# Kernel tuning notes

Measured on AMD Instinct MI355X. Metric: run time of the kernel, lower is better.

The kernel has to match this reference:

```python
import jax, jax.numpy as jnp
import numpy as np

B, S, V, HD, HID, ND = 32, 32, 100, 32, 64, 10


def setup_inputs() -> dict:
    key = jax.random.key(0)
    ks = jax.random.split(key, 32)
    gaps = jax.random.uniform(ks[0], (B, S), jnp.float32) * 0.1 + 0.01
    batch_train_time = jnp.cumsum(gaps, axis=1)                      # sorted event times
    batch_train_type = jax.random.randint(ks[1], (B, S), 0, V)       # event marks in [0, V)
    batch_train_mask = jnp.ones((B, S), jnp.float32)

    def lin(k, i, o):
        return jax.random.normal(k, (i, o), jnp.float32) * (1.0 / np.sqrt(i))

    inp = dict(batch_train_time=batch_train_time,
               batch_train_type=batch_train_type,
               batch_train_mask=batch_train_mask,
               logits=jnp.zeros((2, V * V), jnp.float32),            # torch init: zeros
               h0=jax.random.normal(ks[2], (V, HD), jnp.float32) * 0.01,
               # drift f: in = h_dim + diff_t + last_t
               fW1=lin(ks[3], HD + 2, HID), fb1=jnp.zeros((HID,)),
               fW2=lin(ks[4], HID, HID), fb2=jnp.zeros((HID,)),
               fW3=lin(ks[5], HID, HD), fb3=jnp.zeros((HD,)),
               # diffusion g: in = h_dim + diff_t
               gW1=lin(ks[6], HD + 1, HID), gb1=jnp.zeros((HID,)),
               gW2=lin(ks[7], HID, HID), gb2=jnp.zeros((HID,)),
               gW3=lin(ks[8], HID, HD), gb3=jnp.zeros((HD,)),
               # intensity e: h -> softplus scalar per vertex
               eW1=lin(ks[9], HD, HID), eb1=jnp.zeros((HID,)),
               eW2=lin(ks[10], HID, 1), eb2=jnp.zeros((1,)),
               # jump h
               jW1=lin(ks[11], HD, HID), jb1=jnp.zeros((HID,)),
               jW2=lin(ks[12], HID, HD), jb2=jnp.zeros((HD,)),
               # A_MSG edge mlp: [h_send, h_recv] -> message
               mW1=lin(ks[13], 2 * HD, HID), mb1=jnp.zeros((HID,)),
               mW2=lin(ks[14], HID, HD), mb2=jnp.zeros((HD,)))
    return inp


def reference(batch_train_time, batch_train_type, batch_train_mask, logits, h0,
              fW1, fb1, fW2, fb2, fW3, fb3,
              gW1, gb1, gW2, gb2, gW3, gb3,
              eW1, eb1, eW2, eb2, jW1, jb1, jW2, jb2, mW1, mb1, mW2, mb2):
    barange = jnp.arange(B)
    edge_prob = jax.nn.softmax(logits, axis=0)[1]  # [V*V], P(edge present)

    def mlp3(x, W1, b1, W2, b2, W3, b3):
        h = jnp.tanh(x @ W1 + b1)
        h = jnp.tanh(h @ W2 + b2)
        return h @ W3 + b3

    def f_drift(h, dft, last):
        return mlp3(jnp.concatenate([h, dft, last], -1), fW1, fb1, fW2, fb2, fW3, fb3)

    def g_diff(h, dft):
        return mlp3(jnp.concatenate([h, dft], -1), gW1, gb1, gW2, gb2, gW3, gb3)

    def e_int(h):  # [B,V,HD] -> [B,V] positive intensity
        return jax.nn.softplus(jnp.tanh(h @ eW1 + eb1) @ eW2 + eb2)[..., 0]

    def jump(h):
        return jnp.tanh(h @ jW1 + jb1) @ jW2 + jb2

    def msg_jump(h, ev):
        # message passing from the event node to every vertex, gated by edge_prob
        send = h[barange, ev]                                          # [B,HD]
        pair = jnp.concatenate([jnp.broadcast_to(send[:, None, :], h.shape), h], -1)
        m = jnp.tanh(pair @ mW1 + mb1) @ mW2 + mb2                     # [B,V,HD]
        p = edge_prob[ev[:, None] * V + jnp.arange(V)[None, :]]        # [B,V]
        h = h + m * p[:, :, None]
        # jump update at the event node
        he = h[barange, ev]
        return h.at[barange, ev].add(jump(he))

    def euler(h, t0, t1, key):
        dt = (t1 - t0) / ND                                            # [B]
        dtb = dt[:, None, None]
        l_init = e_int(h)

        def step(carry, j):
            h, k = carry
            k, sub = jax.random.split(k)
            noise = jax.random.normal(sub, h.shape, h.dtype)
            dft = jnp.broadcast_to(dtb * (j + 1.0), (B, V, 1))
            last = jnp.broadcast_to(t0[:, None, None], (B, V, 1))
            h = h + f_drift(h, dft, last) * dtb + g_diff(h, dft) * jnp.sqrt(dtb) * noise
            return (h, k), e_int(h)

        (h, key), ls = jax.lax.scan(step, (h, key), jnp.arange(ND, dtype=jnp.float32))
        l_ts = jnp.concatenate([l_init[:, :, None], jnp.moveaxis(ls, 0, 2)], axis=2)  # [B,V,ND+1]
        ts = t0[:, None] + dt[:, None] * jnp.arange(ND + 1, dtype=dt.dtype)           # [B,ND+1]
        return h, key, ts, l_ts

    # t = 0: initial intensity + first jump
    h = jnp.broadcast_to(h0[None], (B, V, HD))
    l0 = e_int(h)
    ev0 = batch_train_type[:, 0]
    lt0 = l0[barange, ev0]
    h = msg_jump(h, ev0)
    key = jax.random.key(42)

    def interval(carry, xs):
        h, key = carry
        t0, t1, ev = xs
        h, key, ts, l_ts = euler(h, t0, t1, key)
        l_last = l_ts[:, :, -1]                 # pre-jump (left) intensities
        lt = l_last[barange, ev]
        h = msg_jump(h, ev)
        return (h, key), (ts, l_ts, l_last, lt)

    xs = (batch_train_time[:, :-1].T, batch_train_time[:, 1:].T, batch_train_type[:, 1:].T)
    (_h, _k), (ts_all, lts_all, llast_all, lt_all) = jax.lax.scan(interval, (h, key), xs)

    tsave = jnp.moveaxis(ts_all, 0, 1).reshape(B, -1)                       # [B,(S-1)*(ND+1)]
    a_l_tsave = jnp.transpose(lts_all, (1, 2, 0, 3)).reshape(B, V, -1)      # [B,V,(S-1)*(ND+1)]
    a_l_batch_l = jnp.concatenate([l0[:, None, :], jnp.moveaxis(llast_all, 0, 1)], axis=1)  # [B,S,V]
    a_l_time_l = jnp.concatenate([lt0[:, None], lt_all.T], axis=1)          # [B,S]

    sum_term = jnp.sum(jnp.log(a_l_time_l + 1e-16) * batch_train_mask)
    em = jnp.repeat(batch_train_mask[:, 1:], ND + 1, axis=1)                # [B,(S-1)*(ND+1)]
    em = jnp.broadcast_to(em[:, None, :], a_l_tsave.shape)
    lts = a_l_tsave * em
    dts = jnp.diff(tsave, axis=1)[:, None, :]
    integral = jnp.sum((lts[:, :, :-1] * em[:, :, :-1] + lts[:, :, 1:] * em[:, :, 1:])
                       * (dts * em[:, :, 1:])) / 2
    a_nll = integral - sum_term
    return a_nll, a_l_batch_l
```

## Files before the change

### kernel.cpp

```cpp
#include <hip/hip_runtime.h>
#include <hip/hip_fp16.h>
#include <stdint.h>

#define B_  32
#define S_  32
#define V_  100
#define HD_ 32
#define HID_ 64
#define ND_ 10
#define NROW (B_*V_)
#define NTILE 7
#define NBLK (B_*NTILE)
#define NFRAG 58

#define WO_EP    14848
#define WO_HA    24848
#define WO_HB    127248
#define WO_ACC   229648
#define WO_PREVL 232848
#define WO_PREVT 236048
#define WO_LTLOG 239248
#define WO_NOISE 240272
#define NOISE_FLOATS ((size_t)310 * NBLK * 64 * 8)

typedef __attribute__((ext_vector_type(8))) _Float16 f16x8;
typedef __attribute__((ext_vector_type(4))) float f32x4;

#define LGKM_FENCE asm volatile("s_waitcnt lgkmcnt(0)" ::: "memory")

__host__ __device__ inline void tf2x32(uint32_t k0, uint32_t k1,
                                       uint32_t& x0, uint32_t& x1) {
  uint32_t ks0 = k0, ks1 = k1, ks2 = k0 ^ k1 ^ 0x1BD11BDAu;
#define TFR(r) { x0 += x1; x1 = (x1 << (r)) | (x1 >> (32 - (r))); x1 ^= x0; }
  x0 += ks0; x1 += ks1;
  TFR(13) TFR(15) TFR(26) TFR(6)
  x0 += ks1; x1 += ks2 + 1u;
  TFR(17) TFR(29) TFR(16) TFR(24)
  x0 += ks2; x1 += ks0 + 2u;
  TFR(13) TFR(15) TFR(26) TFR(6)
  x0 += ks0; x1 += ks1 + 3u;
  TFR(17) TFR(29) TFR(16) TFR(24)
  x0 += ks1; x1 += ks2 + 4u;
  TFR(13) TFR(15) TFR(26) TFR(6)
  x0 += ks2; x1 += ks0 + 5u;
#undef TFR
}

__device__ __forceinline__ float erfinv_f(float x) {
  float w = -log1pf(-x * x);
  float p;
  if (w < 5.0f) {
    w -= 2.5f;
    p = 2.81022636e-08f;
    p = fmaf(p, w, 3.43273939e-07f);
    p = fmaf(p, w, -3.5233877e-06f);
    p = fmaf(p, w, -4.39150654e-06f);
    p = fmaf(p, w, 0.00021858087f);
    p = fmaf(p, w, -0.00125372503f);
    p = fmaf(p, w, -0.00417768164f);
    p = fmaf(p, w, 0.246640727f);
    p = fmaf(p, w, 1.50140941f);
  } else {
    w = sqrtf(w) - 3.0f;
    p = -0.000200214257f;
    p = fmaf(p, w, 0.000100950558f);
    p = fmaf(p, w, 0.00134934322f);
    p = fmaf(p, w, -0.00367342844f);
    p = fmaf(p, w, 0.00573950773f);
    p = fmaf(p, w, -0.0076224613f);
    p = fmaf(p, w, 0.00943887047f);
    p = fmaf(p, w, 1.00167406f);
    p = fmaf(p, w, 2.83297682f);
  }
  return p * x;
}

__device__ __forceinline__ float tanh_e(float x) {
  float e = __builtin_amdgcn_exp2f(x * 2.885390082f);
  return 1.0f - 2.0f * __builtin_amdgcn_rcpf(e + 1.0f);
}
__device__ __forceinline__ float softplus_fast(float x) {
  return fmaxf(x, 0.0f) + __logf(1.0f + __expf(-fabsf(x)));
}
__device__ __forceinline__ unsigned short f16b(float x) {
  __half h = __float2half(x);
  return *reinterpret_cast<unsigned short*>(&h);
}
__device__ __forceinline__ uint32_t pk2(float a, float b) {
  return (uint32_t)f16b(a) | ((uint32_t)f16b(b) << 16);
}
__device__ __forceinline__ f32x4 MF(f16x8 a, f16x8 b, f32x4 c) {
  return __builtin_amdgcn_mfma_f32_16x16x32_f16(a, b, c, 0, 0, 0);
}

struct SubK { uint32_t k[ND_][2]; };
struct AllK { uint32_t k[310][2]; };

__device__ __forceinline__ void noise8(int row0, int lane, uint32_t k0, uint32_t k1,
                                       float* n) {
  int g = lane >> 4, li = lane & 15;
#pragma unroll
  for (int v = 0; v < 8; ++v) {
    int reg = v & 3, t = v >> 2;
    int row = row0 + 4 * g + reg;
    uint32_t x0 = 0u, x1 = (uint32_t)(row * HD_ + li + 16 * t);
    tf2x32(k0, k1, x0, x1);
    uint32_t bits = x0 ^ x1;
    float fr = __uint_as_float(0x3f800000u | (bits >> 9)) - 1.0f;
    const float LOW = -0.99999994f;
    float u = fmaxf(LOW, fr * 2.0f + LOW);
    n[v] = 1.4142135f * erfinv_f(u);
  }
}

__global__ void prep_k(const float* __restrict__ fW1, const float* __restrict__ gW1,
                       const float* __restrict__ fW2, const float* __restrict__ gW2,
                       const float* __restrict__ fW3, const float* __restrict__ gW3,
                       const float* __restrict__ eW1, const float* __restrict__ eW2,
                       const float* __restrict__ mW1, const float* __restrict__ mW2,
                       const float* __restrict__ jW1, const float* __restrict__ jW2,
                       const float* __restrict__ logits, float* __restrict__ ws) {
  int tid = blockIdx.x * 256 + threadIdx.x;
  if (tid < NFRAG * 64) {
    int fid = tid >> 6, lane = tid & 63;
    int g = lane >> 4, li = lane & 15;
    const float* src; int k0 = 0, n0 = 0, ncol = HID_; bool hperm = false, col0 = false;
    if (fid < 4)       { src = fW1; n0 = 16 * fid;       hperm = true; }
    else if (fid < 8)  { src = gW1; n0 = 16 * (fid - 4); hperm = true; }
    else if (fid < 16) { int q = fid - 8;  src = fW2; n0 = 16 * (q >> 1); k0 = 32 * (q & 1); }
    else if (fid < 24) { int q = fid - 16; src = gW2; n0 = 16 * (q >> 1); k0 = 32 * (q & 1); }
    else if (fid < 28) { int q = fid - 24; src = fW3; n0 = 16 * (q >> 1); k0 = 32 * (q & 1); ncol = HD_; }
    else if (fid < 32) { int q = fid - 28; src = gW3; n0 = 16 * (q >> 1); k0 = 32 * (q & 1); ncol = HD_; }
    else if (fid < 36) { src = eW1; n0 = 16 * (fid - 32); hperm = true; }
    else if (fid < 38) { src = eW2; k0 = 32 * (fid - 36); col0 = true; }
    else if (fid < 46) { int q = fid - 38; src = mW1; k0 = 32 * (q >> 2); n0 = 16 * (q & 3); hperm = true; }
    else if (fid < 50) { int q = fid - 46; src = mW2; k0 = 32 * (q >> 1); n0 = 16 * (q & 1); ncol = HD_; }
    else if (fid < 54) { src = jW1; n0 = 16 * (fid - 50); hperm = true; }
    else               { int q = fid - 54; src = jW2; k0 = 32 * (q >> 1); n0 = 16 * (q & 1); ncol = HD_; }
    unsigned short v[8];
#pragma unroll
    for (int j = 0; j < 8; ++j) {
      int sl = 8 * g + j;
      int k;
      if (hperm) k = k0 + ((sl >> 1) + 16 * (sl & 1));
      else { int s2 = k0 + sl; k = (s2 >> 2) + 16 * (s2 & 3); }
      float x;
      if (col0) x = (li == 0) ? src[k] : 0.0f;
      else      x = src[k * ncol + (n0 + li)];
      v[j] = f16b(x);
    }
    uint4 o;
    o.x = (uint32_t)v[0] | ((uint32_t)v[1] << 16);
    o.y = (uint32_t)v[2] | ((uint32_t)v[3] << 16);
    o.z = (uint32_t)v[4] | ((uint32_t)v[5] << 16);
    o.w = (uint32_t)v[6] | ((uint32_t)v[7] << 16);
    ((uint4*)ws)[fid * 64 + lane] = o;
  } else if (tid < NFRAG * 64 + V_ * V_) {
    int idx = tid - NFRAG * 64;
    float l0v = logits[idx], l1v = logits[V_ * V_ + idx];
    float mx = fmaxf(l0v, l1v);
    float e0 = expf(l0v - mx), e1 = expf(l1v - mx);
    ws[WO_EP + idx] = e1 / (e0 + e1);
  }
}

__global__ void noise_k(float* __restrict__ np, AllK ak) {
  int pair = blockIdx.x * 4 + (threadIdx.x >> 6);
  int lane = threadIdx.x & 63;
  int sg = pair / NBLK, bid = pair - sg * NBLK;
  int b = bid / NTILE, tile = bid - b * NTILE;
  int row0 = b * V_ + tile * 16;
  float n[8];
  noise8(row0, lane, ak.k[sg][0], ak.k[sg][1], n);
  float* dst = np + ((size_t)pair * 64 + lane) * 8;
  f32x4 a = {n[0], n[1], n[2], n[3]}, c = {n[4], n[5], n[6], n[7]};
  ((f32x4*)dst)[0] = a;
  ((f32x4*)dst)[1] = c;
}

template<int K4, int O>
__device__ __forceinline__ float dotWxT(const float* __restrict__ W,
                                        const float* __restrict__ x,
                                        float a, int lane) {
#pragma unroll
  for (int kb = 0; kb < K4; ++kb) {
    float4 xv = *(const float4*)(x + kb * 4);
    a = fmaf(xv.x, W[(kb * 4 + 0) * O + lane], a);
    a = fmaf(xv.y, W[(kb * 4 + 1) * O + lane], a);
    a = fmaf(xv.z, W[(kb * 4 + 2) * O + lane], a);
    a = fmaf(xv.w, W[(kb * 4 + 3) * O + lane], a);
  }
  return a;
}

__launch_bounds__(256)
__global__ void init_k(const int* __restrict__ type_, const float* __restrict__ mask_,
                       const float* __restrict__ h0,
                       const float* __restrict__ eW1, const float* __restrict__ eb1,
                       const float* __restrict__ eW2, const float* __restrict__ eb2,
                       float* __restrict__ hA, float* __restrict__ acc,
                       float* __restrict__ ltlog, float* __restrict__ dout) {
  __shared__ float xls[4][64];
  const int w = threadIdx.x >> 6, lane = threadIdx.x & 63;
  const int row = blockIdx.x * 4 + w;
  const int b = row / V_, v = row - b * V_;
  if (lane < 32) {
    float x = h0[v * HD_ + lane];
    xls[w][lane] = x;
    hA[row * HD_ + lane] = x;
  }
  float a = dotWxT<8, 64>(eW1, xls[w], eb1[lane], lane);
  float t = tanhf(a) * eW2[lane];
#pragma unroll
  for (int o = 1; o < 64; o <<= 1) t += __shfl_xor(t, o, 64);
  float z = t + eb2[0];
  float l0 = fmaxf(z, 0.0f) + log1pf(expf(-fabsf(z)));
  if (lane == 0) {
    dout[1 + (b * S_ + 0) * V_ + v] = l0;
    acc[row] = 0.0f;
    if (v == type_[b * S_]) ltlog[b] = logf(l0 + 1e-16f) * mask_[b * S_];
  }
}

__launch_bounds__(64, 1)
__global__ void euler_k(const float* __restrict__ time_, const int* __restrict__ type_,
                        const float* __restrict__ mask_, const float* __restrict__ wsf,
                        const float* __restrict__ fb1, const float* __restrict__ fb2,
                        const float* __restrict__ fb3, const float* __restrict__ gb1,
                        const float* __restrict__ gb2, const float* __restrict__ gb3,
                        const float* __restrict__ eb1, const float* __restrict__ eb2,
                        const float* __restrict__ eW2, const float* __restrict__ fW1,
                        const float* __restrict__ gW1,
                        const float* __restrict__ mb1, const float* __restrict__ mb2,
                        const float* __restrict__ jb1, const float* __restrict__ jb2,
                        const float* __restrict__ hsrc, float* __restrict__ hdst,
                        float* __restrict__ acc, float* __restrict__ prevl,
                        float* __restrict__ prevt, float* __restrict__ ltlog,
                        float* __restrict__ dout,
                        const float* __restrict__ nin, int s, SubK skc) {
  __shared__ unsigned short actF[16 * 72];
  __shared__ unsigned short actG[16 * 72];
  __shared__ unsigned short hTl[16 * 40];
  __shared__ f16x8 wl[12 * 64];

  const int lane = threadIdx.x;
  const int g = lane >> 4, li = lane & 15;
  const int bid = blockIdx.x;
  const int b = bid / NTILE, tile = bid - b * NTILE;
  const int row0 = b * V_ + tile * 16;
  const int rmax = b * V_ + (V_ - 1);
  const int ev = type_[b * S_ + s - 1];

  const f16x8* WBv = (const f16x8*)wsf;
  const float* ep = wsf + WO_EP;

#pragma unroll
  for (int i = 0; i < 8; ++i) wl[i * 64 + lane] = WBv[i * 64 + lane];
#pragma unroll
  for (int i = 0; i < 4; ++i) wl[(8 + i) * 64 + lane] = WBv[(32 + i) * 64 + lane];

  f16x8 w2f[8], w2g[8], w3f[4], w3g[4];
#pragma unroll
  for (int i = 0; i < 8; ++i) w2f[i] = WBv[(8 + i) * 64 + lane];
#pragma unroll
  for (int i = 0; i < 8; ++i) w2g[i] = WBv[(16 + i) * 64 + lane];
#pragma unroll
  for (int i = 0; i < 4; ++i) w3f[i] = WBv[(24 + i) * 64 + lane];
#pragma unroll
  for (int i = 0; i < 4; ++i) w3g[i] = WBv[(28 + i) * 64 + lane];

  float fb1v[4], gb1v[4], fb2v[4], gb2v[4], eb1v[4], e2v[4], fw32[4], fw33[4], gw32[4];
  float mb1v[4], jb1v[4];
#pragma unroll
  for (int nt = 0; nt < 4; ++nt) {
    int n = li + 16 * nt;
    fb1v[nt] = fb1[n]; gb1v[nt] = gb1[n];
    fb2v[nt] = fb2[n]; gb2v[nt] = gb2[n];
    eb1v[nt] = eb1[n]; e2v[nt] = eW2[n];
    fw32[nt] = fW1[32 * HID_ + n]; fw33[nt] = fW1[33 * HID_ + n];
    gw32[nt] = gW1[32 * HID_ + n];
    mb1v[nt] = mb1[n]; jb1v[nt] = jb1[n];
  }
  float fb3v[2], gb3v[2], mb2v[2], jb2v[2];
#pragma unroll
  for (int nt = 0; nt < 2; ++nt) {
    fb3v[nt] = fb3[li + 16 * nt]; gb3v[nt] = gb3[li + 16 * nt];
    mb2v[nt] = mb2[li + 16 * nt]; jb2v[nt] = jb2[li + 16 * nt];
  }
  const float eb2v = eb2[0];

  const float t0 = time_[b * S_ + s - 1], t1 = time_[b * S_ + s];
  const float dt = (t1 - t0) / 10.0f;
  const float sq = sqrtf(dt);
  const float msk = mask_[b * S_ + s], mskp = mask_[b * S_ + s - 1];

  float hv[2][4];
#pragma unroll
  for (int t = 0; t < 2; ++t)
#pragma unroll
    for (int reg = 0; reg < 4; ++reg) {
      int rv = row0 + 4 * g + reg; if (rv > rmax) rv = rmax;
      hv[t][reg] = hsrc[rv * HD_ + li + 16 * t];
    }

  {
    float sd0 = hsrc[(b * V_ + ev) * HD_ + li];
    float sd1 = hsrc[(b * V_ + ev) * HD_ + li + 16];
    uint32_t su = pk2(sd0, sd1);
#pragma unroll
    for (int reg = 0; reg < 4; ++reg) {
      *(uint32_t*)&actF[(4 * g + reg) * 72 + 2 * li] = su;
      *(uint32_t*)&actG[(4 * g + reg) * 72 + 2 * li] = pk2(hv[0][reg], hv[1][reg]);
    }
    LGKM_FENCE;
    f16x8 ap0 = *(const f16x8*)&actF[li * 72 + 8 * g];
    f16x8 ap1 = *(const f16x8*)&actG[li * 72 + 8 * g];
    f32x4 cm[4];
#pragma unroll
    for (int nt = 0; nt < 4; ++nt) {
      f32x4 c = {mb1v[nt], mb1v[nt], mb1v[nt], mb1v[nt]};
      c = MF(ap0, WBv[(38 + nt) * 64 + lane], c);
      cm[nt] = MF(ap1, WBv[(42 + nt) * 64 + lane], c);
    }
#pragma unroll
    for (int reg = 0; reg < 4; ++reg) {
      uint2 u;
      u.x = pk2(tanh_e(cm[0][reg]), tanh_e(cm[1][reg]));
      u.y = pk2(tanh_e(cm[2][reg]), tanh_e(cm[3][reg]));
      *(uint2*)&actF[(4 * g + reg) * 72 + 4 * li] = u;
    }
    LGKM_FENCE;
    f16x8 am0 = *(const f16x8*)&actF[li * 72 + 8 * g];
    f16x8 am1 = *(const f16x8*)&actF[li * 72 + 32 + 8 * g];
    f32x4 mm[2];
#pragma unroll
    for (int nt = 0; nt < 2; ++nt) {
      f32x4 c = {mb2v[nt], mb2v[nt], mb2v[nt], mb2v[nt]};
      c = MF(am0, WBv[(46 + nt) * 64 + lane], c);
      mm[nt] = MF(am1, WBv[(48 + nt) * 64 + lane], c);
    }
#pragma unroll
    for (int reg = 0; reg < 4; ++reg) {
      int v = tile * 16 + 4 * g + reg; int vc = (v < V_) ? v : (V_ - 1);
      float p = ep[ev * V_ + vc];
      hv[0][reg] += mm[0][reg] * p;
      hv[1][reg] += mm[1][reg] * p;
    }
    if (tile == (ev >> 4)) {
#pragma unroll
      for (int reg = 0; reg < 4; ++reg)
        *(uint32_t*)&hTl[(4 * g + reg) * 40 + 2 * li] = pk2(hv[0][reg], hv[1][reg]);
      LGKM_FENCE;
      f16x8 ah = *(const f16x8*)&hTl[li * 40 + 8 * g];
      f32x4 cj[4];
#pragma unroll
      for (int nt = 0; nt < 4; ++nt) {
        f32x4 c = {jb1v[nt], jb1v[nt], jb1v[nt], jb1v[nt]};
        cj[nt] = MF(ah, WBv[(50 + nt) * 64 + lane], c);
      }
#pragma unroll
      for (int reg = 0; reg < 4; ++reg) {
        uint2 u;
        u.x = pk2(tanh_e(cj[0][reg]), tanh_e(cj[1][reg]));
        u.y = pk2(tanh_e(cj[2][reg]), tanh_e(cj[3][reg]));
        *(uint2*)&actG[(4 * g + reg) * 72 + 4 * li] = u;
      }
      LGKM_FENCE;
      f16x8 aj0 = *(const f16x8*)&actG[li * 72 + 8 * g];
      f16x8 aj1 = *(const f16x8*)&actG[li * 72 + 32 + 8 * g];
      f32x4 jm[2];
#pragma unroll
      for (int nt = 0; nt < 2; ++nt) {
        f32x4 c = {jb2v[nt], jb2v[nt], jb2v[nt], jb2v[nt]};
        c = MF(aj0, WBv[(54 + nt) * 64 + lane], c);
        jm[nt] = MF(aj1, WBv[(56 + nt) * 64 + lane], c);
      }
#pragma unroll
      for (int reg = 0; reg < 4; ++reg)
        if (tile * 16 + 4 * g + reg == ev) {
          hv[0][reg] += jm[0][reg];
          hv[1][reg] += jm[1][reg];
        }
    }
#pragma unroll
    for (int reg = 0; reg < 4; ++reg)
      *(uint32_t*)&hTl[(4 * g + reg) * 40 + 2 * li] = pk2(hv[0][reg], hv[1][reg]);
    LGKM_FENCE;
  }

  float accv[4], lprev[4], plv[4];
#pragma unroll
  for (int reg = 0; reg < 4; ++reg) {
    int rv = row0 + 4 * g + reg; if (rv > rmax) rv = rmax;
    accv[reg] = acc[rv];
    plv[reg] = (s > 1) ? prevl[rv] : 0.0f;
  }
  const float ptv = (s > 1) ? prevt[row0] : 0.0f;

  auto efin = [&](f32x4* ce, float* lout) {
#pragma unroll
    for (int reg = 0; reg < 4; ++reg) {
      float p = tanh_e(ce[0][reg]) * e2v[0];
      p = fmaf(tanh_e(ce[1][reg]), e2v[1], p);
      p = fmaf(tanh_e(ce[2][reg]), e2v[2], p);
      p = fmaf(tanh_e(ce[3][reg]), e2v[3], p);
#pragma unroll
      for (int m = 1; m < 16; m <<= 1) p += __shfl_xor(p, m, 64);
      lout[reg] = softplus_fast(p + eb2v);
    }
  };

#pragma unroll 1
  for (int j = 0; j < ND_; ++j) {
    f32x4 q0, q1;
    if (nin) {
      const float* qp = nin + ((size_t)(j * NBLK + bid) * 64 + lane) * 8;
      q0 = ((const f32x4*)qp)[0]; q1 = ((const f32x4*)qp)[1];
    } else {
      float n[8];
      noise8(row0, lane, skc.k[j][0], skc.k[j][1], n);
      q0 = {n[0], n[1], n[2], n[3]}; q1 = {n[4], n[5], n[6], n[7]};
    }

    f16x8 ah = *(const f16x8*)&hTl[li * 40 + 8 * g];
    f32x4 cf[4], cg[4], ce[4];
#pragma unroll
    for (int nt = 0; nt < 4; ++nt) {
      f32x4 c0 = {fb1v[nt], fb1v[nt], fb1v[nt], fb1v[nt]};
      cf[nt] = MF(ah, wl[nt * 64 + lane], c0);
      f32x4 c1 = {gb1v[nt], gb1v[nt], gb1v[nt], gb1v[nt]};
      cg[nt] = MF(ah, wl[(4 + nt) * 64 + lane], c1);
      f32x4 c2 = {eb1v[nt], eb1v[nt], eb1v[nt], eb1v[nt]};
      ce[nt] = MF(ah, wl[(8 + nt) * 64 + lane], c2);
    }
    const float dft = dt * (float)(j + 1);
    float addf[4], addg[4];
#pragma unroll
    for (int nt = 0; nt < 4; ++nt) {
      addf[nt] = dft * fw32[nt] + t0 * fw33[nt];
      addg[nt] = dft * gw32[nt];
    }
#pragma unroll
    for (int reg = 0; reg < 4; ++reg) {
      uint2 uf, ug;
      uf.x = pk2(tanh_e(cf[0][reg] + addf[0]), tanh_e(cf[1][reg] + addf[1]));
      uf.y = pk2(tanh_e(cf[2][reg] + addf[2]), tanh_e(cf[3][reg] + addf[3]));
      *(uint2*)&actF[(4 * g + reg) * 72 + 4 * li] = uf;
      ug.x = pk2(tanh_e(cg[0][reg] + addg[0]), tanh_e(cg[1][reg] + addg[1]));
      ug.y = pk2(tanh_e(cg[2][reg] + addg[2]), tanh_e(cg[3][reg] + addg[3]));
      *(uint2*)&actG[(4 * g + reg) * 72 + 4 * li] = ug;
    }
    float lc[4];
    efin(ce, lc);
    if (j == 0) {
      if (s > 1) {
#pragma unroll
        for (int reg = 0; reg < 4; ++reg)
          accv[reg] += (plv[reg] * mskp + lc[reg] * msk) * (t0 - ptv) * msk;
      }
    } else {
      float dtm = dt * msk;
#pragma unroll
      for (int reg = 0; reg < 4; ++reg)
        accv[reg] += (lprev[reg] * msk + lc[reg] * msk) * dtm;
    }
#pragma unroll
    for (int reg = 0; reg < 4; ++reg) lprev[reg] = lc[reg];
    LGKM_FENCE;
    f16x8 af0 = *(const f16x8*)&actF[li * 72 + 8 * g];
    f16x8 af1 = *(const f16x8*)&actF[li * 72 + 32 + 8 * g];
    f16x8 ag0 = *(const f16x8*)&actG[li * 72 + 8 * g];
    f16x8 ag1 = *(const f16x8*)&actG[li * 72 + 32 + 8 * g];
#pragma unroll
    for (int nt = 0; nt < 4; ++nt) {
      f32x4 c = {fb2v[nt], fb2v[nt], fb2v[nt], fb2v[nt]};
      c = MF(af0, w2f[2 * nt], c);
      cf[nt] = MF(af1, w2f[2 * nt + 1], c);
      f32x4 d = {gb2v[nt], gb2v[nt], gb2v[nt], gb2v[nt]};
      d = MF(ag0, w2g[2 * nt], d);
      cg[nt] = MF(ag1, w2g[2 * nt + 1], d);
    }
#pragma unroll
    for (int reg = 0; reg < 4; ++reg) {
      uint2 uf, ug;
      uf.x = pk2(tanh_e(cf[0][reg]), tanh_e(cf[1][reg]));
      uf.y = pk2(tanh_e(cf[2][reg]), tanh_e(cf[3][reg]));
      *(uint2*)&actF[(4 * g + reg) * 72 + 4 * li] = uf;
      ug.x = pk2(tanh_e(cg[0][reg]), tanh_e(cg[1][reg]));
      ug.y = pk2(tanh_e(cg[2][reg]), tanh_e(cg[3][reg]));
      *(uint2*)&actG[(4 * g + reg) * 72 + 4 * li] = ug;
    }
    LGKM_FENCE;
    af0 = *(const f16x8*)&actF[li * 72 + 8 * g];
    af1 = *(const f16x8*)&actF[li * 72 + 32 + 8 * g];
    ag0 = *(const f16x8*)&actG[li * 72 + 8 * g];
    ag1 = *(const f16x8*)&actG[li * 72 + 32 + 8 * g];
    f32x4 dr[2], di[2];
#pragma unroll
    for (int nt = 0; nt < 2; ++nt) {
      f32x4 c = {fb3v[nt], fb3v[nt], fb3v[nt], fb3v[nt]};
      c = MF(af0, w3f[2 * nt], c);
      dr[nt] = MF(af1, w3f[2 * nt + 1], c);
      f32x4 d = {gb3v[nt], gb3v[nt], gb3v[nt], gb3v[nt]};
      d = MF(ag0, w3g[2 * nt], d);
      di[nt] = MF(ag1, w3g[2 * nt + 1], d);
    }
#pragma unroll
    for (int reg = 0; reg < 4; ++reg) {
      hv[0][reg] += dr[0][reg] * dt + di[0][reg] * sq * q0[reg];
      hv[1][reg] += dr[1][reg] * dt + di[1][reg] * sq * q1[reg];
    }
#pragma unroll
    for (int reg = 0; reg < 4; ++reg)
      *(uint32_t*)&hTl[(4 * g + reg) * 40 + 2 * li] = pk2(hv[0][reg], hv[1][reg]);
    LGKM_FENCE;
  }

  float llast[4];
  {
    f16x8 ah = *(const f16x8*)&hTl[li * 40 + 8 * g];
    f32x4 ce[4];
#pragma unroll
    for (int nt = 0; nt < 4; ++nt) {
      f32x4 c = {eb1v[nt], eb1v[nt], eb1v[nt], eb1v[nt]};
      ce[nt] = MF(ah, wl[(8 + nt) * 64 + lane], c);
    }
    efin(ce, llast);
    float dtm = dt * msk;
#pragma unroll
    for (int reg = 0; reg < 4; ++reg)
      accv[reg] += (lprev[reg] * msk + llast[reg] * msk) * dtm;
  }

#pragma unroll
  for (int t = 0; t < 2; ++t)
#pragma unroll
    for (int reg = 0; reg < 4; ++reg) {
      int v = tile * 16 + 4 * g + reg;
      if (v < V_) hdst[(row0 + 4 * g + reg) * HD_ + li + 16 * t] = hv[t][reg];
    }
  if (li == 0) {
    int evn = type_[b * S_ + s];
    float pt = t0 + dt * 10.0f;
#pragma unroll
    for (int reg = 0; reg < 4; ++reg) {
      int v = tile * 16 + 4 * g + reg;
      if (v < V_) {
        int rv = row0 + 4 * g + reg;
        acc[rv] = accv[reg];
        prevl[rv] = llast[reg];
        prevt[rv] = pt;
        dout[1 + (b * S_ + s) * V_ + v] = llast[reg];
        if (v == evn) ltlog[s * B_ + b] = logf(llast[reg] + 1e-16f) * msk;
      }
    }
  }
}

__global__ void reduce_k(const float* __restrict__ acc, const float* __restrict__ ltlog,
                         float* __restrict__ dout) {
  __shared__ double sh[512];
  int t = threadIdx.x;
  double ia = 0.0, st = 0.0;
  for (int i = t; i < NROW; i += 256) ia += (double)acc[i];
  for (int i = t; i < B_ * S_; i += 256) st += (double)ltlog[i];
  sh[t] = ia; sh[256 + t] = st;
  __syncthreads();
  for (int o = 128; o > 0; o >>= 1) {
    if (t < o) { sh[t] += sh[t + o]; sh[256 + t] += sh[256 + t + o]; }
    __syncthreads();
  }
  if (t == 0) dout[0] = (float)(0.5 * sh[0] - sh[256]);
}

extern "C" void kernel_launch(void* const* d_in, const int* in_sizes, int n_in,
                              void* d_out, int out_size, void* d_ws, size_t ws_size,
                              hipStream_t stream) {
  const float* time_  = (const float*)d_in[0];
  const int*   type_  = (const int*)d_in[1];
  const float* mask_  = (const float*)d_in[2];
  const float* logits = (const float*)d_in[3];
  const float* h0     = (const float*)d_in[4];
  const float* fW1 = (const float*)d_in[5];  const float* fb1 = (const float*)d_in[6];
  const float* fW2 = (const float*)d_in[7];  const float* fb2 = (const float*)d_in[8];
  const float* fW3 = (const float*)d_in[9];  const float* fb3 = (const float*)d_in[10];
  const float* gW1 = (const float*)d_in[11]; const float* gb1 = (const float*)d_in[12];
  const float* gW2 = (const float*)d_in[13]; const float* gb2 = (const float*)d_in[14];
  const float* gW3 = (const float*)d_in[15]; const float* gb3 = (const float*)d_in[16];
  const float* eW1 = (const float*)d_in[17]; const float* eb1 = (const float*)d_in[18];
  const float* eW2 = (const float*)d_in[19]; const float* eb2 = (const float*)d_in[20];
  const float* jW1 = (const float*)d_in[21]; const float* jb1 = (const float*)d_in[22];
  const float* jW2 = (const float*)d_in[23]; const float* jb2 = (const float*)d_in[24];
  const float* mW1 = (const float*)d_in[25]; const float* mb1 = (const float*)d_in[26];
  const float* mW2 = (const float*)d_in[27]; const float* mb2 = (const float*)d_in[28];
  float* out = (float*)d_out;

  float* ws    = (float*)d_ws;
  float* hA    = ws + WO_HA;
  float* hB    = ws + WO_HB;
  float* acc   = ws + WO_ACC;
  float* prevl = ws + WO_PREVL;
  float* prevt = ws + WO_PREVT;
  float* ltlog = ws + WO_LTLOG;

  uint32_t kh = 0u, kl = 42u;
  AllK ak;
  for (int n = 0; n < 310; ++n) {
    uint32_t a0 = 0u, a1 = 0u; tf2x32(kh, kl, a0, a1);
    uint32_t b0 = 0u, b1 = 1u; tf2x32(kh, kl, b0, b1);
    ak.k[n][0] = b0; ak.k[n][1] = b1;
    kh = a0; kl = a1;
  }

  const bool useNoise = ws_size >= ((size_t)WO_NOISE + NOISE_FLOATS) * 4;
  float* noisep = useNoise ? (ws + WO_NOISE) : nullptr;

  prep_k<<<54, 256, 0, stream>>>(fW1, gW1, fW2, gW2, fW3, gW3, eW1, eW2,
                                 mW1, mW2, jW1, jW2, logits, ws);
  init_k<<<NROW / 4, 256, 0, stream>>>(type_, mask_, h0, eW1, eb1, eW2, eb2,
                                       hA, acc, ltlog, out);
  if (useNoise)
    noise_k<<<(310 * NBLK) / 4, 256, 0, stream>>>(noisep, ak);

  for (int s = 1; s <= 31; ++s) {
    const float* hs = (s & 1) ? hA : hB;
    float*       hd = (s & 1) ? hB : hA;
    SubK skc;
    for (int j = 0; j < ND_; ++j) {
      skc.k[j][0] = ak.k[(s - 1) * ND_ + j][0];
      skc.k[j][1] = ak.k[(s - 1) * ND_ + j][1];
    }
    const float* nin = useNoise ? (noisep + (size_t)(s - 1) * ND_ * NBLK * 64 * 8) : nullptr;
    euler_k<<<NBLK, 64, 0, stream>>>(time_, type_, mask_, ws,
                                     fb1, fb2, fb3, gb1, gb2, gb3, eb1, eb2, eW2,
                                     fW1, gW1, mb1, mb2, jb1, jb2,
                                     hs, hd, acc, prevl, prevt, ltlog, out,
                                     nin, s, skc);
  }
  reduce_k<<<1, 256, 0, stream>>>(acc, ltlog, out);
}
```

Baseline: 1.119 ms.

## Split drift and diffusion MLPs across two waves and generate noise inline

Each euler block now runs two wavefronts: wave 0 evaluates the drift MLP and owns the state update, and wave 1 evaluates the diffusion MLP plus the intensity head and accumulation. Diffusion outputs pass to wave 0 through shared memory, with block barriers each Euler substep. The precomputed noise buffer and its kernel are removed; each wave computes its half of the Threefry/erfinv noise inline. This halves per-wave MFMA and tanh work on the serial critical path, at the cost of two __syncthreads per substep and recomputing RNG inside the timed loop.

```diff
diff --git a/kernel.cpp b/kernel.cpp
--- a/kernel.cpp
+++ b/kernel.cpp
@@ -20,8 +20,6 @@
 #define WO_PREVL 232848
 #define WO_PREVT 236048
 #define WO_LTLOG 239248
-#define WO_NOISE 240272
-#define NOISE_FLOATS ((size_t)310 * NBLK * 64 * 8)
 
 typedef __attribute__((ext_vector_type(8))) _Float16 f16x8;
 typedef __attribute__((ext_vector_type(4))) float f32x4;
@@ -94,14 +92,12 @@
 }
 
 struct SubK { uint32_t k[ND_][2]; };
-struct AllK { uint32_t k[310][2]; };
-
-__device__ __forceinline__ void noise8(int row0, int lane, uint32_t k0, uint32_t k1,
+
+__device__ __forceinline__ void noise4(int row0, int lane, int t, uint32_t k0, uint32_t k1,
                                        float* n) {
   int g = lane >> 4, li = lane & 15;
 #pragma unroll
-  for (int v = 0; v < 8; ++v) {
-    int reg = v & 3, t = v >> 2;
+  for (int reg = 0; reg < 4; ++reg) {
     int row = row0 + 4 * g + reg;
     uint32_t x0 = 0u, x1 = (uint32_t)(row * HD_ + li + 16 * t);
     tf2x32(k0, k1, x0, x1);
@@ -109,7 +105,7 @@
     float fr = __uint_as_float(0x3f800000u | (bits >> 9)) - 1.0f;
     const float LOW = -0.99999994f;
     float u = fmaxf(LOW, fr * 2.0f + LOW);
-    n[v] = 1.4142135f * erfinv_f(u);
+    n[reg] = 1.4142135f * erfinv_f(u);
   }
 }
 
@@ -164,20 +160,6 @@
   }
 }
 
-__global__ void noise_k(float* __restrict__ np, AllK ak) {
-  int pair = blockIdx.x * 4 + (threadIdx.x >> 6);
-  int lane = threadIdx.x & 63;
-  int sg = pair / NBLK, bid = pair - sg * NBLK;
-  int b = bid / NTILE, tile = bid - b * NTILE;
-  int row0 = b * V_ + tile * 16;
-  float n[8];
-  noise8(row0, lane, ak.k[sg][0], ak.k[sg][1], n);
-  float* dst = np + ((size_t)pair * 64 + lane) * 8;
-  f32x4 a = {n[0], n[1], n[2], n[3]}, c = {n[4], n[5], n[6], n[7]};
-  ((f32x4*)dst)[0] = a;
-  ((f32x4*)dst)[1] = c;
-}
-
 template<int K4, int O>
 __device__ __forceinline__ float dotWxT(const float* __restrict__ W,
                                         const float* __restrict__ x,
@@ -222,7 +204,7 @@
   }
 }
 
-__launch_bounds__(64, 1)
+__launch_bounds__(128, 1)
 __global__ void euler_k(const float* __restrict__ time_, const int* __restrict__ type_,
                         const float* __restrict__ mask_, const float* __restrict__ wsf,
                         const float* __restrict__ fb1, const float* __restrict__ fb2,
@@ -236,14 +218,16 @@
                         const float* __restrict__ hsrc, float* __restrict__ hdst,
                         float* __restrict__ acc, float* __restrict__ prevl,
                         float* __restrict__ prevt, float* __restrict__ ltlog,
-                        float* __restrict__ dout,
-                        const float* __restrict__ nin, int s, SubK skc) {
+                        float* __restrict__ dout, int s, SubK skc) {
   __shared__ unsigned short actF[16 * 72];
   __shared__ unsigned short actG[16 * 72];
   __shared__ unsigned short hTl[16 * 40];
-  __shared__ f16x8 wl[12 * 64];
-
-  const int lane = threadIdx.x;
+  __shared__ float4 dtA[64];
+  __shared__ float4 dtB[64];
+
+  const int wv = threadIdx.x >> 6;
+  const bool w1 = (wv == 1);
+  const int lane = threadIdx.x & 63;
   const int g = lane >> 4, li = lane & 15;
   const int bid = blockIdx.x;
   const int b = bid / NTILE, tile = bid - b * NTILE;
@@ -254,37 +238,32 @@
   const f16x8* WBv = (const f16x8*)wsf;
   const float* ep = wsf + WO_EP;
 
-#pragma unroll
-  for (int i = 0; i < 8; ++i) wl[i * 64 + lane] = WBv[i * 64 + lane];
-#pragma unroll
-  for (int i = 0; i < 4; ++i) wl[(8 + i) * 64 + lane] = WBv[(32 + i) * 64 + lane];
-
-  f16x8 w2f[8], w2g[8], w3f[4], w3g[4];
-#pragma unroll
-  for (int i = 0; i < 8; ++i) w2f[i] = WBv[(8 + i) * 64 + lane];
-#pragma unroll
-  for (int i = 0; i < 8; ++i) w2g[i] = WBv[(16 + i) * 64 + lane];
-#pragma unroll
-  for (int i = 0; i < 4; ++i) w3f[i] = WBv[(24 + i) * 64 + lane];
-#pragma unroll
-  for (int i = 0; i < 4; ++i) w3g[i] = WBv[(28 + i) * 64 + lane];
-
-  float fb1v[4], gb1v[4], fb2v[4], gb2v[4], eb1v[4], e2v[4], fw32[4], fw33[4], gw32[4];
-  float mb1v[4], jb1v[4];
+  const int o1 = w1 ? 4 : 0, o2 = w1 ? 16 : 8, o3 = w1 ? 28 : 24;
+  f16x8 wA[4], wB[8], wC[4], wE[4];
+#pragma unroll
+  for (int i = 0; i < 4; ++i) wA[i] = WBv[(o1 + i) * 64 + lane];
+#pragma unroll
+  for (int i = 0; i < 8; ++i) wB[i] = WBv[(o2 + i) * 64 + lane];
+#pragma unroll
+  for (int i = 0; i < 4; ++i) wC[i] = WBv[(o3 + i) * 64 + lane];
+#pragma unroll
+  for (int i = 0; i < 4; ++i) wE[i] = WBv[(32 + i) * 64 + lane];
+
+  float b1v[4], b2v[4], aw0[4], aw1[4], eb1v[4], e2v[4], mb1v[4], jb1v[4];
 #pragma unroll
   for (int nt = 0; nt < 4; ++nt) {
     int n = li + 16 * nt;
-    fb1v[nt] = fb1[n]; gb1v[nt] = gb1[n];
-    fb2v[nt] = fb2[n]; gb2v[nt] = gb2[n];
+    b1v[nt] = w1 ? gb1[n] : fb1[n];
+    b2v[nt] = w1 ? gb2[n] : fb2[n];
+    aw0[nt] = w1 ? gW1[32 * HID_ + n] : fW1[32 * HID_ + n];
+    aw1[nt] = w1 ? 0.0f : fW1[33 * HID_ + n];
     eb1v[nt] = eb1[n]; e2v[nt] = eW2[n];
-    fw32[nt] = fW1[32 * HID_ + n]; fw33[nt] = fW1[33 * HID_ + n];
-    gw32[nt] = gW1[32 * HID_ + n];
     mb1v[nt] = mb1[n]; jb1v[nt] = jb1[n];
   }
-  float fb3v[2], gb3v[2], mb2v[2], jb2v[2];
+  float b3v[2], mb2v[2], jb2v[2];
 #pragma unroll
   for (int nt = 0; nt < 2; ++nt) {
-    fb3v[nt] = fb3[li + 16 * nt]; gb3v[nt] = gb3[li + 16 * nt];
+    b3v[nt] = w1 ? gb3[li + 16 * nt] : fb3[li + 16 * nt];
     mb2v[nt] = mb2[li + 16 * nt]; jb2v[nt] = jb2[li + 16 * nt];
   }
   const float eb2v = eb2[0];
@@ -295,15 +274,15 @@
   const float msk = mask_[b * S_ + s], mskp = mask_[b * S_ + s - 1];
 
   float hv[2][4];
-#pragma unroll
-  for (int t = 0; t < 2; ++t)
-#pragma unroll
-    for (int reg = 0; reg < 4; ++reg) {
-      int rv = row0 + 4 * g + reg; if (rv > rmax) rv = rmax;
-      hv[t][reg] = hsrc[rv * HD_ + li + 16 * t];
-    }
-
-  {
+
+  if (!w1) {
+#pragma unroll
+    for (int t = 0; t < 2; ++t)
+#pragma unroll
+      for (int reg = 0; reg < 4; ++reg) {
+        int rv = row0 + 4 * g + reg; if (rv > rmax) rv = rmax;
+        hv[t][reg] = hsrc[rv * HD_ + li + 16 * t];
+      }
     float sd0 = hsrc[(b * V_ + ev) * HD_ + li];
     float sd1 = hsrc[(b * V_ + ev) * HD_ + li + 16];
     uint32_t su = pk2(sd0, sd1);
@@ -385,17 +364,19 @@
 #pragma unroll
     for (int reg = 0; reg < 4; ++reg)
       *(uint32_t*)&hTl[(4 * g + reg) * 40 + 2 * li] = pk2(hv[0][reg], hv[1][reg]);
-    LGKM_FENCE;
-  }
-
-  float accv[4], lprev[4], plv[4];
-#pragma unroll
-  for (int reg = 0; reg < 4; ++reg) {
-    int rv = row0 + 4 * g + reg; if (rv > rmax) rv = rmax;
-    accv[reg] = acc[rv];
-    plv[reg] = (s > 1) ? prevl[rv] : 0.0f;
-  }
-  const float ptv = (s > 1) ? prevt[row0] : 0.0f;
+  }
+
+  float accv[4] = {0.f, 0.f, 0.f, 0.f}, lprev[4], plv[4] = {0.f, 0.f, 0.f, 0.f};
+  float ptv = 0.0f;
+  if (w1) {
+#pragma unroll
+    for (int reg = 0; reg < 4; ++reg) {
+      int rv = row0 + 4 * g + reg; if (rv > rmax) rv = rmax;
+      accv[reg] = acc[rv];
+      plv[reg] = (s > 1) ? prevl[rv] : 0.0f;
+    }
+    ptv = (s > 1) ? prevt[row0] : 0.0f;
+  }
 
   auto efin = [&](f32x4* ce, float* lout) {
 #pragma unroll
@@ -410,150 +391,148 @@
     }
   };
 
+  __syncthreads();
+
+  unsigned short* act = w1 ? actG : actF;
+
 #pragma unroll 1
   for (int j = 0; j < ND_; ++j) {
-    f32x4 q0, q1;
-    if (nin) {
-      const float* qp = nin + ((size_t)(j * NBLK + bid) * 64 + lane) * 8;
-      q0 = ((const f32x4*)qp)[0]; q1 = ((const f32x4*)qp)[1];
-    } else {
-      float n[8];
-      noise8(row0, lane, skc.k[j][0], skc.k[j][1], n);
-      q0 = {n[0], n[1], n[2], n[3]}; q1 = {n[4], n[5], n[6], n[7]};
-    }
-
-    f16x8 ah = *(const f16x8*)&hTl[li * 40 + 8 * g];
-    f32x4 cf[4], cg[4], ce[4];
-#pragma unroll
-    for (int nt = 0; nt < 4; ++nt) {
-      f32x4 c0 = {fb1v[nt], fb1v[nt], fb1v[nt], fb1v[nt]};
-      cf[nt] = MF(ah, wl[nt * 64 + lane], c0);
-      f32x4 c1 = {gb1v[nt], gb1v[nt], gb1v[nt], gb1v[nt]};
-      cg[nt] = MF(ah, wl[(4 + nt) * 64 + lane], c1);
-      f32x4 c2 = {eb1v[nt], eb1v[nt], eb1v[nt], eb1v[nt]};
-      ce[nt] = MF(ah, wl[(8 + nt) * 64 + lane], c2);
-    }
-    const float dft = dt * (float)(j + 1);
-    float addf[4], addg[4];
-#pragma unroll
-    for (int nt = 0; nt < 4; ++nt) {
-      addf[nt] = dft * fw32[nt] + t0 * fw33[nt];
-      addg[nt] = dft * gw32[nt];
-    }
-#pragma unroll
-    for (int reg = 0; reg < 4; ++reg) {
-      uint2 uf, ug;
-      uf.x = pk2(tanh_e(cf[0][reg] + addf[0]), tanh_e(cf[1][reg] + addf[1]));
-      uf.y = pk2(tanh_e(cf[2][reg] + addf[2]), tanh_e(cf[3][reg] + addf[3]));
-      *(uint2*)&actF[(4 * g + reg) * 72 + 4 * li] = uf;
-      ug.x = pk2(tanh_e(cg[0][reg] + addg[0]), tanh_e(cg[1][reg] + addg[1]));
-      ug.y = pk2(tanh_e(cg[2][reg] + addg[2]), tanh_e(cg[3][reg] + addg[3]));
-      *(uint2*)&actG[(4 * g + reg) * 72 + 4 * li] = ug;
-    }
-    float lc[4];
-    efin(ce, lc);
-    if (j == 0) {
-      if (s > 1) {
-#pragma unroll
-        for (int reg = 0; reg < 4; ++reg)
-          accv[reg] += (plv[reg] * mskp + lc[reg] * msk) * (t0 - ptv) * msk;
-      }
-    } else {
-      float dtm = dt * msk;
-#pragma unroll
-      for (int reg = 0; reg < 4; ++reg)
-        accv[reg] += (lprev[reg] * msk + lc[reg] * msk) * dtm;
-    }
-#pragma unroll
-    for (int reg = 0; reg < 4; ++reg) lprev[reg] = lc[reg];
-    LGKM_FENCE;
-    f16x8 af0 = *(const f16x8*)&actF[li * 72 + 8 * g];
-    f16x8 af1 = *(const f16x8*)&actF[li * 72 + 32 + 8 * g];
-    f16x8 ag0 = *(const f16x8*)&actG[li * 72 + 8 * g];
-    f16x8 ag1 = *(const f16x8*)&actG[li * 72 + 32 + 8 * g];
-#pragma unroll
-    for (int nt = 0; nt < 4; ++nt) {
-      f32x4 c = {fb2v[nt], fb2v[nt], fb2v[nt], fb2v[nt]};
-      c = MF(af0, w2f[2 * nt], c);
-      cf[nt] = MF(af1, w2f[2 * nt + 1], c);
-      f32x4 d = {gb2v[nt], gb2v[nt], gb2v[nt], gb2v[nt]};
-      d = MF(ag0, w2g[2 * nt], d);
-      cg[nt] = MF(ag1, w2g[2 * nt + 1], d);
-    }
-#pragma unroll
-    for (int reg = 0; reg < 4; ++reg) {
-      uint2 uf, ug;
-      uf.x = pk2(tanh_e(cf[0][reg]), tanh_e(cf[1][reg]));
-      uf.y = pk2(tanh_e(cf[2][reg]), tanh_e(cf[3][reg]));
-      *(uint2*)&actF[(4 * g + reg) * 72 + 4 * li] = uf;
-      ug.x = pk2(tanh_e(cg[0][reg]), tanh_e(cg[1][reg]));
-      ug.y = pk2(tanh_e(cg[2][reg]), tanh_e(cg[3][reg]));
-      *(uint2*)&actG[(4 * g + reg) * 72 + 4 * li] = ug;
-    }
-    LGKM_FENCE;
-    af0 = *(const f16x8*)&actF[li * 72 + 8 * g];
-    af1 = *(const f16x8*)&actF[li * 72 + 32 + 8 * g];
-    ag0 = *(const f16x8*)&actG[li * 72 + 8 * g];
-    ag1 = *(const f16x8*)&actG[li * 72 + 32 + 8 * g];
-    f32x4 dr[2], di[2];
-#pragma unroll
-    for (int nt = 0; nt < 2; ++nt) {
-      f32x4 c = {fb3v[nt], fb3v[nt], fb3v[nt], fb3v[nt]};
-      c = MF(af0, w3f[2 * nt], c);
-      dr[nt] = MF(af1, w3f[2 * nt + 1], c);
-      f32x4 d = {gb3v[nt], gb3v[nt], gb3v[nt], gb3v[nt]};
-      d = MF(ag0, w3g[2 * nt], d);
-      di[nt] = MF(ag1, w3g[2 * nt + 1], d);
-    }
-#pragma unroll
-    for (int reg = 0; reg < 4; ++reg) {
-      hv[0][reg] += dr[0][reg] * dt + di[0][reg] * sq * q0[reg];
-      hv[1][reg] += dr[1][reg] * dt + di[1][reg] * sq * q1[reg];
-    }
-#pragma unroll
-    for (int reg = 0; reg < 4; ++reg)
-      *(uint32_t*)&hTl[(4 * g + reg) * 40 + 2 * li] = pk2(hv[0][reg], hv[1][reg]);
-    LGKM_FENCE;
-  }
-
-  float llast[4];
-  {
+    float nzh[4];
+    noise4(row0, lane, wv, skc.k[j][0], skc.k[j][1], nzh);
+
     f16x8 ah = *(const f16x8*)&hTl[li * 40 + 8 * g];
     f32x4 ce[4];
+    if (w1) {
+#pragma unroll
+      for (int nt = 0; nt < 4; ++nt) {
+        f32x4 c = {eb1v[nt], eb1v[nt], eb1v[nt], eb1v[nt]};
+        ce[nt] = MF(ah, wE[nt], c);
+      }
+    }
+    f32x4 c1[4];
+#pragma unroll
+    for (int nt = 0; nt < 4; ++nt) {
+      f32x4 c = {b1v[nt], b1v[nt], b1v[nt], b1v[nt]};
+      c1[nt] = MF(ah, wA[nt], c);
+    }
+    const float dft = dt * (float)(j + 1);
+    float addv[4];
+#pragma unroll
+    for (int nt = 0; nt < 4; ++nt) addv[nt] = dft * aw0[nt] + t0 * aw1[nt];
+#pragma unroll
+    for (int reg = 0; reg < 4; ++reg) {
+      uint2 u;
+      u.x = pk2(tanh_e(c1[0][reg] + addv[0]), tanh_e(c1[1][reg] + addv[1]));
+      u.y = pk2(tanh_e(c1[2][reg] + addv[2]), tanh_e(c1[3][reg] + addv[3]));
+      *(uint2*)&act[(4 * g + reg) * 72 + 4 * li] = u;
+    }
+    if (w1) {
+      float lc[4];
+      efin(ce, lc);
+      if (j == 0) {
+        if (s > 1) {
+#pragma unroll
+          for (int reg = 0; reg < 4; ++reg)
+            accv[reg] += (plv[reg] * mskp + lc[reg] * msk) * (t0 - ptv) * msk;
+        }
+      } else {
+        float dtm = dt * msk;
+#pragma unroll
+        for (int reg = 0; reg < 4; ++reg)
+          accv[reg] += (lprev[reg] * msk + lc[reg] * msk) * dtm;
+      }
+#pragma unroll
+      for (int reg = 0; reg < 4; ++reg) lprev[reg] = lc[reg];
+    }
+    LGKM_FENCE;
+    f16x8 a0 = *(const f16x8*)&act[li * 72 + 8 * g];
+    f16x8 a1 = *(const f16x8*)&act[li * 72 + 32 + 8 * g];
+    f32x4 c2[4];
+#pragma unroll
+    for (int nt = 0; nt < 4; ++nt) {
+      f32x4 c = {b2v[nt], b2v[nt], b2v[nt], b2v[nt]};
+      c = MF(a0, wB[2 * nt], c);
+      c2[nt] = MF(a1, wB[2 * nt + 1], c);
+    }
+#pragma unroll
+    for (int reg = 0; reg < 4; ++reg) {
+      uint2 u;
+      u.x = pk2(tanh_e(c2[0][reg]), tanh_e(c2[1][reg]));
+      u.y = pk2(tanh_e(c2[2][reg]), tanh_e(c2[3][reg]));
+      *(uint2*)&act[(4 * g + reg) * 72 + 4 * li] = u;
+    }
+    LGKM_FENCE;
+    a0 = *(const f16x8*)&act[li * 72 + 8 * g];
+    a1 = *(const f16x8*)&act[li * 72 + 32 + 8 * g];
+    f32x4 o3[2];
+#pragma unroll
+    for (int nt = 0; nt < 2; ++nt) {
+      f32x4 c = {b3v[nt], b3v[nt], b3v[nt], b3v[nt]};
+      c = MF(a0, wC[2 * nt], c);
+      o3[nt] = MF(a1, wC[2 * nt + 1], c);
+    }
+    if (w1) {
+      float4 da; da.x = o3[0][0]; da.y = o3[0][1]; da.z = o3[0][2]; da.w = o3[0][3];
+      float4 db; db.x = o3[1][0] * sq * nzh[0]; db.y = o3[1][1] * sq * nzh[1];
+      db.z = o3[1][2] * sq * nzh[2]; db.w = o3[1][3] * sq * nzh[3];
+      dtA[lane] = da; dtB[lane] = db;
+    }
+    __syncthreads();
+    if (!w1) {
+      float4 da = dtA[lane], db = dtB[lane];
+      hv[0][0] += o3[0][0] * dt + da.x * sq * nzh[0];
+      hv[0][1] += o3[0][1] * dt + da.y * sq * nzh[1];
+      hv[0][2] += o3[0][2] * dt + da.z * sq * nzh[2];
+      hv[0][3] += o3[0][3] * dt + da.w * sq * nzh[3];
+      hv[1][0] += o3[1][0] * dt + db.x;
+      hv[1][1] += o3[1][1] * dt + db.y;
+      hv[1][2] += o3[1][2] * dt + db.z;
+      hv[1][3] += o3[1][3] * dt + db.w;
+#pragma unroll
+      for (int reg = 0; reg < 4; ++reg)
+        *(uint32_t*)&hTl[(4 * g + reg) * 40 + 2 * li] = pk2(hv[0][reg], hv[1][reg]);
+    }
+    __syncthreads();
+  }
+
+  if (w1) {
+    float llast[4];
+    f16x8 ah = *(const f16x8*)&hTl[li * 40 + 8 * g];
+    f32x4 ce[4];
 #pragma unroll
     for (int nt = 0; nt < 4; ++nt) {
       f32x4 c = {eb1v[nt], eb1v[nt], eb1v[nt], eb1v[nt]};
-      ce[nt] = MF(ah, wl[(8 + nt) * 64 + lane], c);
+      ce[nt] = MF(ah, wE[nt], c);
     }
     efin(ce, llast);
     float dtm = dt * msk;
 #pragma unroll
     for (int reg = 0; reg < 4; ++reg)
       accv[reg] += (lprev[reg] * msk + llast[reg] * msk) * dtm;
-  }
-
-#pragma unroll
-  for (int t = 0; t < 2; ++t)
-#pragma unroll
-    for (int reg = 0; reg < 4; ++reg) {
-      int v = tile * 16 + 4 * g + reg;
-      if (v < V_) hdst[(row0 + 4 * g + reg) * HD_ + li + 16 * t] = hv[t][reg];
-    }
-  if (li == 0) {
-    int evn = type_[b * S_ + s];
-    float pt = t0 + dt * 10.0f;
-#pragma unroll
-    for (int reg = 0; reg < 4; ++reg) {
-      int v = tile * 16 + 4 * g + reg;
-      if (v < V_) {
-        int rv = row0 + 4 * g + reg;
-        acc[rv] = accv[reg];
-        prevl[rv] = llast[reg];
-        prevt[rv] = pt;
-        dout[1 + (b * S_ + s) * V_ + v] = llast[reg];
-        if (v == evn) ltlog[s * B_ + b] = logf(llast[reg] + 1e-16f) * msk;
-      }
-    }
+    if (li == 0) {
+      int evn = type_[b * S_ + s];
+      float pt = t0 + dt * 10.0f;
+#pragma unroll
+      for (int reg = 0; reg < 4; ++reg) {
+        int v = tile * 16 + 4 * g + reg;
+        if (v < V_) {
+          int rv = row0 + 4 * g + reg;
+          acc[rv] = accv[reg];
+          prevl[rv] = llast[reg];
+          prevt[rv] = pt;
+          dout[1 + (b * S_ + s) * V_ + v] = llast[reg];
+          if (v == evn) ltlog[s * B_ + b] = logf(llast[reg] + 1e-16f) * msk;
+        }
+      }
+    }
+  } else {
+#pragma unroll
+    for (int t = 0; t < 2; ++t)
+#pragma unroll
+      for (int reg = 0; reg < 4; ++reg) {
+        int v = tile * 16 + 4 * g + reg;
+        if (v < V_) hdst[(row0 + 4 * g + reg) * HD_ + li + 16 * t] = hv[t][reg];
+      }
   }
 }
 
@@ -604,38 +583,32 @@
   float* ltlog = ws + WO_LTLOG;
 
   uint32_t kh = 0u, kl = 42u;
-  AllK ak;
+  uint32_t subs[310][2];
   for (int n = 0; n < 310; ++n) {
     uint32_t a0 = 0u, a1 = 0u; tf2x32(kh, kl, a0, a1);
     uint32_t b0 = 0u, b1 = 1u; tf2x32(kh, kl, b0, b1);
-    ak.k[n][0] = b0; ak.k[n][1] = b1;
+    subs[n][0] = b0; subs[n][1] = b1;
     kh = a0; kl = a1;
   }
-
-  const bool useNoise = ws_size >= ((size_t)WO_NOISE + NOISE_FLOATS) * 4;
-  float* noisep = useNoise ? (ws + WO_NOISE) : nullptr;
 
   prep_k<<<54, 256, 0, stream>>>(fW1, gW1, fW2, gW2, fW3, gW3, eW1, eW2,
                                  mW1, mW2, jW1, jW2, logits, ws);
   init_k<<<NROW / 4, 256, 0, stream>>>(type_, mask_, h0, eW1, eb1, eW2, eb2,
                                        hA, acc, ltlog, out);
-  if (useNoise)
-    noise_k<<<(310 * NBLK) / 4, 256, 0, stream>>>(noisep, ak);
 
   for (int s = 1; s <= 31; ++s) {
     const float* hs = (s & 1) ? hA : hB;
     float*       hd = (s & 1) ? hB : hA;
     SubK skc;
     for (int j = 0; j < ND_; ++j) {
-      skc.k[j][0] = ak.k[(s - 1) * ND_ + j][0];
-      skc.k[j][1] = ak.k[(s - 1) * ND_ + j][1];
-    }
-    const float* nin = useNoise ? (noisep + (size_t)(s - 1) * ND_ * NBLK * 64 * 8) : nullptr;
-    euler_k<<<NBLK, 64, 0, stream>>>(time_, type_, mask_, ws,
-                                     fb1, fb2, fb3, gb1, gb2, gb3, eb1, eb2, eW2,
-                                     fW1, gW1, mb1, mb2, jb1, jb2,
-                                     hs, hd, acc, prevl, prevt, ltlog, out,
-                                     nin, s, skc);
+      skc.k[j][0] = subs[(s - 1) * ND_ + j][0];
+      skc.k[j][1] = subs[(s - 1) * ND_ + j][1];
+    }
+    euler_k<<<NBLK, 128, 0, stream>>>(time_, type_, mask_, ws,
+                                      fb1, fb2, fb3, gb1, gb2, gb3, eb1, eb2, eW2,
+                                      fW1, gW1, mb1, mb2, jb1, jb2,
+                                      hs, hd, acc, prevl, prevt, ltlog, out,
+                                      s, skc);
   }
   reduce_k<<<1, 256, 0, stream>>>(acc, ltlog, out);
 }
```

Result: slower. 1.242 ms (+11.0%).
